# Kernel tuning notes

Measured on AMD Instinct MI355X. Metric: run time of the kernel, lower is better.

The kernel has to match this reference:

```python
import jax, jax.numpy as jnp
import numpy as np

REG_MAX = 16
BOX_W = 7.5
OBJ_W = 1.0
TOPK = 10
EPS = 1e-7


def dfl_decode(x, reg_max):
    # x: [B, 4*reg_max, N] -> expected value of per-side distribution -> [B, N, 4] (xyxy)
    B, C, N = x.shape
    x = x.reshape(B, 4, reg_max, N)
    p = jax.nn.softmax(x, axis=2)
    proj = jnp.arange(reg_max, dtype=x.dtype)
    return jnp.einsum('bkrn,r->bnk', p, proj)


def bbox_ciou(b1, b2):
    # b1: [B,N,1,4], b2: [B,1,M,4], xyxy -> [B,N,M]
    x11, y11, x12, y12 = b1[..., 0], b1[..., 1], b1[..., 2], b1[..., 3]
    x21, y21, x22, y22 = b2[..., 0], b2[..., 1], b2[..., 2], b2[..., 3]
    w1, h1 = x12 - x11, y12 - y11
    w2, h2 = x22 - x21, y22 - y21
    iw = jnp.clip(jnp.minimum(x12, x22) - jnp.maximum(x11, x21), 0.0)
    ih = jnp.clip(jnp.minimum(y12, y22) - jnp.maximum(y11, y21), 0.0)
    inter = iw * ih
    union = w1 * h1 + w2 * h2 - inter + EPS
    iou = inter / union
    cw = jnp.maximum(x12, x22) - jnp.minimum(x11, x21)
    ch = jnp.maximum(y12, y22) - jnp.minimum(y11, y21)
    c2 = cw * cw + ch * ch + EPS
    rho2 = ((x21 + x22 - x11 - x12) ** 2 + (y21 + y22 - y11 - y12) ** 2) * 0.25
    v = (4.0 / (np.pi ** 2)) * (jnp.arctan(w2 / (h2 + EPS)) - jnp.arctan(w1 / (h1 + EPS))) ** 2
    alpha = jax.lax.stop_gradient(v / (v - iou + 1.0 + EPS))
    return iou - rho2 / c2 - alpha * v


def setup_inputs() -> dict:
    key = jax.random.key(0)
    k1, k2, k3, k4 = jax.random.split(key, 4)
    B, N, M = 8, 34000, 64
    boxes = jax.random.normal(k1, (B, 4 * REG_MAX, N), dtype=jnp.float32)
    scores = jax.random.normal(k2, (B, N), dtype=jnp.float32)
    # GT boxes: valid xyxy in roughly the same [0, reg_max) range as decoded preds
    xy = jax.random.uniform(k3, (B, M, 2), dtype=jnp.float32) * 11.0
    wh = jax.random.uniform(k4, (B, M, 2), dtype=jnp.float32) * 4.0 + 0.5
    targets = jnp.concatenate([xy, xy + wh], axis=-1)
    return {'boxes': boxes, 'scores': scores, 'targets': targets}


def reference(boxes, scores, targets):
    B, N = scores.shape
    M = targets.shape[1]
    pb = dfl_decode(boxes, REG_MAX)                     # [B,N,4]
    ciou = bbox_ciou(pb[:, :, None, :], targets[:, None, :, :])  # [B,N,M]
    k = min(TOPK, N)
    topv, topi = jax.lax.top_k(jnp.swapaxes(ciou, 1, 2), k)      # [B,M,k] over anchors
    valid = topv > 0.0
    vals = jnp.where(valid, topv, 0.0)

    def per_batch(idx, val, vld):
        flat_i = idx.reshape(-1)
        iou_t = jnp.zeros((N,), val.dtype).at[flat_i].max(val.reshape(-1))
        pos = jnp.zeros((N,), bool).at[flat_i].max(vld.reshape(-1))
        return iou_t, pos

    iou_target, pos = jax.vmap(per_batch)(topi, vals, valid)     # [B,N]
    posf = pos.astype(iou_target.dtype)
    npos = posf.sum(axis=1)
    box_per = jnp.where(npos > 0,
                        ((1.0 - iou_target) * posf).sum(axis=1) / jnp.maximum(npos, 1.0),
                        0.0)
    box_loss = box_per.sum()
    # BCEWithLogits (mean over anchors), summed over batch
    bce = jnp.maximum(scores, 0.0) - scores * iou_target + jnp.log1p(jnp.exp(-jnp.abs(scores)))
    obj_loss = bce.mean(axis=1).sum()
    total = (BOX_W * box_loss + OBJ_W * obj_loss) / B
    return total, box_loss, obj_loss
```

## Files before the change

### kernel.cpp

```cpp
#include <hip/hip_runtime.h>
#include <math.h>

#define BQ 8
#define MQ 64
#define REGMAX 16
#define KTOP 10
#define EPSQ 1e-7f
#define APB 512
#define MBUF 1024

__device__ __forceinline__ float frcp(float x) { return __builtin_amdgcn_rcpf(x); }

__device__ __forceinline__ float dfl_side(const float* __restrict__ p, size_t Ns) {
  float x0 = p[0];
  float x1 = p[Ns];
  float x2 = p[2 * Ns];
  float x3 = p[3 * Ns];
  float x4 = p[4 * Ns];
  float x5 = p[5 * Ns];
  float x6 = p[6 * Ns];
  float x7 = p[7 * Ns];
  float x8 = p[8 * Ns];
  float x9 = p[9 * Ns];
  float x10 = p[10 * Ns];
  float x11 = p[11 * Ns];
  float x12 = p[12 * Ns];
  float x13 = p[13 * Ns];
  float x14 = p[14 * Ns];
  float x15 = p[15 * Ns];
  float mx = fmaxf(fmaxf(fmaxf(fmaxf(x0, x1), fmaxf(x2, x3)),
                         fmaxf(fmaxf(x4, x5), fmaxf(x6, x7))),
                   fmaxf(fmaxf(fmaxf(x8, x9), fmaxf(x10, x11)),
                         fmaxf(fmaxf(x12, x13), fmaxf(x14, x15))));
  float s = 0.f, ws = 0.f, e;
  e = __expf(x0 - mx); s += e;
  e = __expf(x1 - mx); s += e; ws += 1.f * e;
  e = __expf(x2 - mx); s += e; ws += 2.f * e;
  e = __expf(x3 - mx); s += e; ws += 3.f * e;
  e = __expf(x4 - mx); s += e; ws += 4.f * e;
  e = __expf(x5 - mx); s += e; ws += 5.f * e;
  e = __expf(x6 - mx); s += e; ws += 6.f * e;
  e = __expf(x7 - mx); s += e; ws += 7.f * e;
  e = __expf(x8 - mx); s += e; ws += 8.f * e;
  e = __expf(x9 - mx); s += e; ws += 9.f * e;
  e = __expf(x10 - mx); s += e; ws += 10.f * e;
  e = __expf(x11 - mx); s += e; ws += 11.f * e;
  e = __expf(x12 - mx); s += e; ws += 12.f * e;
  e = __expf(x13 - mx); s += e; ws += 13.f * e;
  e = __expf(x14 - mx); s += e; ws += 14.f * e;
  e = __expf(x15 - mx); s += e; ws += 15.f * e;
  return ws * frcp(s);
}

__device__ __forceinline__ float2 dfl_side2(const float* __restrict__ p, size_t Ns) {
  float2 x0 = *(const float2*)(p);
  float2 x1 = *(const float2*)(p + Ns);
  float2 x2 = *(const float2*)(p + 2 * Ns);
  float2 x3 = *(const float2*)(p + 3 * Ns);
  float2 x4 = *(const float2*)(p + 4 * Ns);
  float2 x5 = *(const float2*)(p + 5 * Ns);
  float2 x6 = *(const float2*)(p + 6 * Ns);
  float2 x7 = *(const float2*)(p + 7 * Ns);
  float2 x8 = *(const float2*)(p + 8 * Ns);
  float2 x9 = *(const float2*)(p + 9 * Ns);
  float2 x10 = *(const float2*)(p + 10 * Ns);
  float2 x11 = *(const float2*)(p + 11 * Ns);
  float2 x12 = *(const float2*)(p + 12 * Ns);
  float2 x13 = *(const float2*)(p + 13 * Ns);
  float2 x14 = *(const float2*)(p + 14 * Ns);
  float2 x15 = *(const float2*)(p + 15 * Ns);
  float mxa = fmaxf(fmaxf(fmaxf(fmaxf(x0.x, x1.x), fmaxf(x2.x, x3.x)),
                          fmaxf(fmaxf(x4.x, x5.x), fmaxf(x6.x, x7.x))),
                    fmaxf(fmaxf(fmaxf(x8.x, x9.x), fmaxf(x10.x, x11.x)),
                          fmaxf(fmaxf(x12.x, x13.x), fmaxf(x14.x, x15.x))));
  float mxb = fmaxf(fmaxf(fmaxf(fmaxf(x0.y, x1.y), fmaxf(x2.y, x3.y)),
                          fmaxf(fmaxf(x4.y, x5.y), fmaxf(x6.y, x7.y))),
                    fmaxf(fmaxf(fmaxf(x8.y, x9.y), fmaxf(x10.y, x11.y)),
                          fmaxf(fmaxf(x12.y, x13.y), fmaxf(x14.y, x15.y))));
  float sa = 0.f, wa = 0.f, sb = 0.f, wb = 0.f, e;
  e = __expf(x0.x - mxa); sa += e;
  e = __expf(x0.y - mxb); sb += e;
  e = __expf(x1.x - mxa); sa += e; wa += 1.f * e;
  e = __expf(x1.y - mxb); sb += e; wb += 1.f * e;
  e = __expf(x2.x - mxa); sa += e; wa += 2.f * e;
  e = __expf(x2.y - mxb); sb += e; wb += 2.f * e;
  e = __expf(x3.x - mxa); sa += e; wa += 3.f * e;
  e = __expf(x3.y - mxb); sb += e; wb += 3.f * e;
  e = __expf(x4.x - mxa); sa += e; wa += 4.f * e;
  e = __expf(x4.y - mxb); sb += e; wb += 4.f * e;
  e = __expf(x5.x - mxa); sa += e; wa += 5.f * e;
  e = __expf(x5.y - mxb); sb += e; wb += 5.f * e;
  e = __expf(x6.x - mxa); sa += e; wa += 6.f * e;
  e = __expf(x6.y - mxb); sb += e; wb += 6.f * e;
  e = __expf(x7.x - mxa); sa += e; wa += 7.f * e;
  e = __expf(x7.y - mxb); sb += e; wb += 7.f * e;
  e = __expf(x8.x - mxa); sa += e; wa += 8.f * e;
  e = __expf(x8.y - mxb); sb += e; wb += 8.f * e;
  e = __expf(x9.x - mxa); sa += e; wa += 9.f * e;
  e = __expf(x9.y - mxb); sb += e; wb += 9.f * e;
  e = __expf(x10.x - mxa); sa += e; wa += 10.f * e;
  e = __expf(x10.y - mxb); sb += e; wb += 10.f * e;
  e = __expf(x11.x - mxa); sa += e; wa += 11.f * e;
  e = __expf(x11.y - mxb); sb += e; wb += 11.f * e;
  e = __expf(x12.x - mxa); sa += e; wa += 12.f * e;
  e = __expf(x12.y - mxb); sb += e; wb += 12.f * e;
  e = __expf(x13.x - mxa); sa += e; wa += 13.f * e;
  e = __expf(x13.y - mxb); sb += e; wb += 13.f * e;
  e = __expf(x14.x - mxa); sa += e; wa += 14.f * e;
  e = __expf(x14.y - mxb); sb += e; wb += 14.f * e;
  e = __expf(x15.x - mxa); sa += e; wa += 15.f * e;
  e = __expf(x15.y - mxb); sb += e; wb += 15.f * e;
  return make_float2(wa * frcp(sa), wb * frcp(sb));
}

__global__ __launch_bounds__(256) void decode_topk_kernel(
    const float* __restrict__ boxes, const float* __restrict__ scores,
    const float* __restrict__ targets, unsigned int* __restrict__ iou_bits,
    uint2* __restrict__ cand, float* __restrict__ bcePartial,
    unsigned int* __restrict__ ctr, int N, int bpb) {
  const int tid = threadIdx.x;
  const int b = blockIdx.x / bpb;
  const int blk = blockIdx.x - b * bpb;
  const int a0 = blk * APB;
  const int w = tid >> 6;
  const int l = tid & 63;

  __shared__ float4 s_sv[APB];
  __shared__ float s_at[APB];
  __shared__ int s_ix[APB];
  __shared__ float s_hv[4 * MQ * KTOP];
  __shared__ int s_hi[4 * MQ * KTOP];
  __shared__ uint2 s_mg[MQ * KTOP];
  __shared__ int s_cnt;
  __shared__ float s_bce;
  if (tid == 0) { s_cnt = 0; s_bce = 0.f; }
  if (blockIdx.x == 0 && tid == 0) *ctr = 0u;
  __syncthreads();

  const int n0 = a0 + 2 * tid;
  float bce0 = 0.f;
  if (n0 < N) {
    const size_t i = (size_t)b * N + n0;
    const size_t Ns = (size_t)N;
    const float* base = boxes + (size_t)(b * 64) * Ns + n0;
    if (n0 + 1 < N) {
      iou_bits[i] = 0u;
      iou_bits[i + 1] = 0u;
      float2 sc = *(const float2*)(scores + i);
      bce0 = fmaxf(sc.x, 0.f) + log1pf(__expf(-fabsf(sc.x))) +
             fmaxf(sc.y, 0.f) + log1pf(__expf(-fabsf(sc.y)));
      float2 ev0 = dfl_side2(base, Ns);
      float2 ev1 = dfl_side2(base + 16 * Ns, Ns);
      float2 ev2 = dfl_side2(base + 32 * Ns, Ns);
      float2 ev3 = dfl_side2(base + 48 * Ns, Ns);
      float w1 = ev2.x - ev0.x, h1 = ev3.x - ev1.x;
      if (w1 > 0.f && h1 > 0.f) {
        int slot = atomicAdd(&s_cnt, 1);
        s_sv[slot] = make_float4(ev0.x, ev1.x, ev2.x, ev3.x);
        s_at[slot] = atanf(w1 * frcp(h1 + EPSQ));
        s_ix[slot] = n0;
      }
      float w1b = ev2.y - ev0.y, h1b = ev3.y - ev1.y;
      if (w1b > 0.f && h1b > 0.f) {
        int slot = atomicAdd(&s_cnt, 1);
        s_sv[slot] = make_float4(ev0.y, ev1.y, ev2.y, ev3.y);
        s_at[slot] = atanf(w1b * frcp(h1b + EPSQ));
        s_ix[slot] = n0 + 1;
      }
    } else {
      iou_bits[i] = 0u;
      float sc = scores[i];
      bce0 = fmaxf(sc, 0.f) + log1pf(__expf(-fabsf(sc)));
      float ev0 = dfl_side(base, Ns);
      float ev1 = dfl_side(base + 16 * Ns, Ns);
      float ev2 = dfl_side(base + 32 * Ns, Ns);
      float ev3 = dfl_side(base + 48 * Ns, Ns);
      float w1 = ev2 - ev0, h1 = ev3 - ev1;
      if (w1 > 0.f && h1 > 0.f) {
        int slot = atomicAdd(&s_cnt, 1);
        s_sv[slot] = make_float4(ev0, ev1, ev2, ev3);
        s_at[slot] = atanf(w1 * frcp(h1 + EPSQ));
        s_ix[slot] = n0;
      }
    }
  }
#pragma unroll
  for (int d = 1; d < 64; d <<= 1) bce0 += __shfl_xor(bce0, d, 64);
  if (l == 0) atomicAdd(&s_bce, bce0);
  __syncthreads();
  const int nsurv = s_cnt;
  if (tid == 0) bcePartial[blockIdx.x] = s_bce;

  const float4 t = ((const float4*)targets)[b * MQ + l];
  const float x21 = t.x, y21 = t.y, x22 = t.z, y22 = t.w;
  const float w2 = x22 - x21, h2 = y22 - y21;
  const float atan_t = atanf(w2 * frcp(h2 + EPSQ));
  const float area2 = w2 * h2, sumx2 = x21 + x22, sumy2 = y21 + y22;
  const float CPI = 4.0f / (float)(M_PI * M_PI);

  float hv0 = 0.f, hv1 = 0.f, hv2 = 0.f, hv3 = 0.f, hv4 = 0.f;
  float hv5 = 0.f, hv6 = 0.f, hv7 = 0.f, hv8 = 0.f, hv9 = 0.f;
  int hi0 = 0, hi1 = 0, hi2 = 0, hi3 = 0, hi4 = 0;
  int hi5 = 0, hi6 = 0, hi7 = 0, hi8 = 0, hi9 = 0;

  const int qlen = (nsurv + 3) >> 2;
  const int j0 = w * qlen;
  const int j1 = min(nsurv, j0 + qlen);
  for (int j = j0; j < j1; ++j) {
    float4 p = s_sv[j];
    float pa = s_at[j];
    int ixj = s_ix[j];
    float x11 = p.x, y11 = p.y, x12 = p.z, y12 = p.w;
    float w1 = x12 - x11, h1 = y12 - y11;
    float iw = fmaxf(fminf(x12, x22) - fmaxf(x11, x21), 0.f);
    float ih = fmaxf(fminf(y12, y22) - fmaxf(y11, y21), 0.f);
    float inter = iw * ih;
    float uni = w1 * h1 + area2 - inter + EPSQ;
    float iou = inter * frcp(uni);
    float cw = fmaxf(x12, x22) - fminf(x11, x21);
    float ch = fmaxf(y12, y22) - fminf(y11, y21);
    float c2 = cw * cw + ch * ch + EPSQ;
    float dx = sumx2 - x11 - x12;
    float dy = sumy2 - y11 - y12;
    float rho2 = (dx * dx + dy * dy) * 0.25f;
    float da = atan_t - pa;
    float v = CPI * da * da;
    float alpha = v * frcp(v - iou + 1.f + EPSQ);
    float ciou = iou - rho2 * frcp(c2) - alpha * v;
    if (ciou > hv9) {
      float cv = ciou;
      int ci = ixj;
#define INS(vk, ik)                         \
  {                                         \
    bool gt = cv > vk;                      \
    float tv_ = vk; int ti_ = ik;           \
    vk = gt ? cv : vk; ik = gt ? ci : ik;   \
    cv = gt ? tv_ : cv; ci = gt ? ti_ : ci; \
  }
      INS(hv0, hi0) INS(hv1, hi1) INS(hv2, hi2) INS(hv3, hi3) INS(hv4, hi4)
      INS(hv5, hi5) INS(hv6, hi6) INS(hv7, hi7) INS(hv8, hi8) INS(hv9, hi9)
#undef INS
    }
  }
  const int hb = (w * MQ + l) * KTOP;
  s_hv[hb + 0] = hv0; s_hi[hb + 0] = hi0;
  s_hv[hb + 1] = hv1; s_hi[hb + 1] = hi1;
  s_hv[hb + 2] = hv2; s_hi[hb + 2] = hi2;
  s_hv[hb + 3] = hv3; s_hi[hb + 3] = hi3;
  s_hv[hb + 4] = hv4; s_hi[hb + 4] = hi4;
  s_hv[hb + 5] = hv5; s_hi[hb + 5] = hi5;
  s_hv[hb + 6] = hv6; s_hi[hb + 6] = hi6;
  s_hv[hb + 7] = hv7; s_hi[hb + 7] = hi7;
  s_hv[hb + 8] = hv8; s_hi[hb + 8] = hi8;
  s_hv[hb + 9] = hv9; s_hi[hb + 9] = hi9;
  __syncthreads();

  if (w == 0) {
    const int m = l;
    int p0 = 0, p1 = 0, p2 = 0, p3 = 0;
    for (int r = 0; r < KTOP; ++r) {
      float c0 = s_hv[(0 * MQ + m) * KTOP + p0];
      float c1 = s_hv[(1 * MQ + m) * KTOP + p1];
      float c2m = s_hv[(2 * MQ + m) * KTOP + p2];
      float c3 = s_hv[(3 * MQ + m) * KTOP + p3];
      float best = c0; int bw = 0;
      if (c1 > best) { best = c1; bw = 1; }
      if (c2m > best) { best = c2m; bw = 2; }
      if (c3 > best) { best = c3; bw = 3; }
      int psel = (bw == 0) ? p0 : (bw == 1) ? p1 : (bw == 2) ? p2 : p3;
      int bidx = s_hi[(bw * MQ + m) * KTOP + psel];
      s_mg[m * KTOP + r] = make_uint2(__float_as_uint(best), (unsigned)bidx);
      if (bw == 0) p0 = min(p0 + 1, KTOP - 1);
      else if (bw == 1) p1 = min(p1 + 1, KTOP - 1);
      else if (bw == 2) p2 = min(p2 + 1, KTOP - 1);
      else p3 = min(p3 + 1, KTOP - 1);
    }
  }
  __syncthreads();
  for (int sl = tid; sl < MQ * KTOP; sl += 256) {
    int m = sl / KTOP;
    int r = sl - m * KTOP;
    cand[((size_t)(b * MQ + m) * bpb + blk) * KTOP + r] = s_mg[sl];
  }
}

__device__ __forceinline__ void select_top10(
    float* s_bv, int* s_bi, float* s_winv, int* s_wini,
    int* s_cnt, int c, int tid) {
  if (tid < 64) {
    for (int r = 0; r < KTOP; ++r) {
      float bv = 0.f;
      int bs = 0xffff;
      for (int sl = tid; sl < c; sl += 64) {
        float v = s_bv[sl];
        if (v > bv) { bv = v; bs = sl; }
      }
      unsigned long long key =
          ((unsigned long long)__float_as_uint(bv) << 32) | (unsigned int)bs;
#pragma unroll
      for (int d = 1; d < 64; d <<= 1) {
        unsigned long long o = __shfl_xor(key, d, 64);
        if (o > key) key = o;
      }
      if (tid == 0) {
        float wv = __uint_as_float((unsigned int)(key >> 32));
        int ws = (int)(key & 0xffffu);
        s_winv[r] = wv;
        if (wv > 0.f && ws != 0xffff) {
          s_wini[r] = s_bi[ws];
          s_bv[ws] = 0.f;
        } else {
          s_wini[r] = 0;
        }
      }
    }
    if (tid < KTOP) { s_bv[tid] = s_winv[tid]; s_bi[tid] = s_wini[tid]; }
    if (tid == 0) *s_cnt = KTOP;
  }
}

__global__ __launch_bounds__(256) void merge_kernel(
    const uint2* __restrict__ cand, const float* __restrict__ scores,
    unsigned int* __restrict__ iou_bits, const float* __restrict__ bcePartial,
    float* __restrict__ mergePartial, unsigned int* __restrict__ ctr,
    float* __restrict__ out, int N, int bpb) {
  const int bm = blockIdx.x;
  const int b = bm >> 6;
  const int tid = threadIdx.x;
  const int NC = bpb * KTOP;

  __shared__ float s_bv[MBUF];
  __shared__ int s_bi[MBUF];
  __shared__ float s_winv[KTOP];
  __shared__ int s_wini[KTOP];
  __shared__ int s_cnt;
  __shared__ float s_d[3];
  __shared__ int s_last;
  __shared__ float s_box[BQ], s_obj[BQ];
  if (tid == 0) s_cnt = 0;
  if (tid < 3) s_d[tid] = 0.f;
  __syncthreads();

  const uint2* cbase = cand + (size_t)bm * NC;
  for (int k2 = tid; k2 < NC; k2 += 256) {
    uint2 e = cbase[k2];
    float v = __uint_as_float(e.x);
    if (v > 0.f) {
      int slot = atomicAdd(&s_cnt, 1);
      s_bv[slot] = v;
      s_bi[slot] = (int)e.y;
    }
  }
  __syncthreads();
  int c = s_cnt;
  __syncthreads();
  if (c > KTOP) {
    select_top10(s_bv, s_bi, s_winv, s_wini, &s_cnt, c, tid);
    __syncthreads();
    c = KTOP;
  }
  if (tid < KTOP && tid < c) {
    float v = s_bv[tid];
    if (v > 0.f) {
      int ix = s_bi[tid];
      unsigned int vb = __float_as_uint(v);
      unsigned int old = atomicMax(&iou_bits[(size_t)b * N + ix], vb);
      if (old < vb) {
        float vold = __uint_as_float(old);
        bool was = (old != 0u);
        atomicAdd(&s_d[0], was ? (vold - v) : (1.f - v));
        if (!was) atomicAdd(&s_d[1], 1.f);
        atomicAdd(&s_d[2], -scores[(size_t)b * N + ix] * (v - vold));
      }
    }
  }
  __syncthreads();
  if (tid == 0) {
    float4* mp = (float4*)(mergePartial + (size_t)bm * 4);
    *mp = make_float4(s_d[0], s_d[1], s_d[2], 0.f);
    __threadfence();
    unsigned int done = atomicAdd(ctr, 1u);
    s_last = (done == (unsigned)(gridDim.x - 1)) ? 1 : 0;
  }
  __syncthreads();
  if (s_last) {
    __threadfence();
    if (tid < BQ) {
      const int bb = tid;
      volatile const float* mp = mergePartial;
      float sbox = 0.f, snp = 0.f, sbce = 0.f;
      for (int mm = 0; mm < MQ; ++mm) {
        int idx = (bb * MQ + mm) * 4;
        sbox += mp[idx];
        snp += mp[idx + 1];
        sbce += mp[idx + 2];
      }
      volatile const float* bp = bcePartial;
      for (int k2 = 0; k2 < bpb; ++k2) sbce += bp[bb * bpb + k2];
      s_box[bb] = (snp > 0.f) ? sbox / fmaxf(snp, 1.f) : 0.f;
      s_obj[bb] = sbce / (float)N;
    }
    __syncthreads();
    if (tid == 0) {
      float box = 0.f, obj = 0.f;
      for (int bb = 0; bb < BQ; ++bb) { box += s_box[bb]; obj += s_obj[bb]; }
      out[0] = (7.5f * box + obj) / (float)BQ;
      out[1] = box;
      out[2] = obj;
    }
  }
}

extern "C" void kernel_launch(void* const* d_in, const int* in_sizes, int n_in,
                              void* d_out, int out_size, void* d_ws, size_t ws_size,
                              hipStream_t stream) {
  const float* boxes = (const float*)d_in[0];
  const float* scores = (const float*)d_in[1];
  const float* targets = (const float*)d_in[2];
  float* out = (float*)d_out;
  const int N = in_sizes[1] / BQ;

  const int bpb = (N + APB - 1) / APB;
  const int nblk = BQ * bpb;

  char* ws = (char*)d_ws;
  size_t cand_bytes = (size_t)BQ * MQ * bpb * KTOP * sizeof(uint2);
  size_t iou_bytes = (size_t)BQ * N * sizeof(unsigned int);
  size_t bce_bytes = (((size_t)nblk * sizeof(float)) + 255) & ~(size_t)255;
  size_t mp_bytes = (size_t)BQ * MQ * 4 * sizeof(float);

  uint2* cand = (uint2*)ws;                    ws += cand_bytes;
  unsigned int* iou_bits = (unsigned int*)ws;  ws += iou_bytes;
  float* bcePartial = (float*)ws;              ws += bce_bytes;
  float* mergePartial = (float*)ws;            ws += mp_bytes;
  unsigned int* ctr = (unsigned int*)ws;

  decode_topk_kernel<<<nblk, 256, 0, stream>>>(boxes, scores, targets,
                                               iou_bits, cand, bcePartial, ctr, N, bpb);
  merge_kernel<<<BQ * MQ, 256, 0, stream>>>(cand, scores, iou_bits, bcePartial,
                                            mergePartial, ctr, out, N, bpb);
}
```

Before: 164.3 us.

## Decode four anchors per thread with float4 loads and parallelize final reduction

Each thread now decodes four consecutive anchors using float4 loads of the DFL logits, which doubles anchors per block and halves the number of blocks and the per-block candidate lists the merge stage scans. The last merge block's final sum over partials is spread across all threads with shared atomics instead of eight serial threads. The trade-off is more registers per thread, which can lower occupancy, plus fewer but heavier blocks and larger top-k candidate sets per block.

New measurement: 159.3 us. 1.03x faster.

```diff
diff --git a/kernel.cpp b/kernel.cpp
--- a/kernel.cpp
+++ b/kernel.cpp
@@ -6,7 +6,7 @@
 #define REGMAX 16
 #define KTOP 10
 #define EPSQ 1e-7f
-#define APB 512
+#define APB 1024
 #define MBUF 1024
 
 __device__ __forceinline__ float frcp(float x) { return __builtin_amdgcn_rcpf(x); }
@@ -52,65 +52,47 @@
   return ws * frcp(s);
 }
 
-__device__ __forceinline__ float2 dfl_side2(const float* __restrict__ p, size_t Ns) {
-  float2 x0 = *(const float2*)(p);
-  float2 x1 = *(const float2*)(p + Ns);
-  float2 x2 = *(const float2*)(p + 2 * Ns);
-  float2 x3 = *(const float2*)(p + 3 * Ns);
-  float2 x4 = *(const float2*)(p + 4 * Ns);
-  float2 x5 = *(const float2*)(p + 5 * Ns);
-  float2 x6 = *(const float2*)(p + 6 * Ns);
-  float2 x7 = *(const float2*)(p + 7 * Ns);
-  float2 x8 = *(const float2*)(p + 8 * Ns);
-  float2 x9 = *(const float2*)(p + 9 * Ns);
-  float2 x10 = *(const float2*)(p + 10 * Ns);
-  float2 x11 = *(const float2*)(p + 11 * Ns);
-  float2 x12 = *(const float2*)(p + 12 * Ns);
-  float2 x13 = *(const float2*)(p + 13 * Ns);
-  float2 x14 = *(const float2*)(p + 14 * Ns);
-  float2 x15 = *(const float2*)(p + 15 * Ns);
-  float mxa = fmaxf(fmaxf(fmaxf(fmaxf(x0.x, x1.x), fmaxf(x2.x, x3.x)),
-                          fmaxf(fmaxf(x4.x, x5.x), fmaxf(x6.x, x7.x))),
-                    fmaxf(fmaxf(fmaxf(x8.x, x9.x), fmaxf(x10.x, x11.x)),
-                          fmaxf(fmaxf(x12.x, x13.x), fmaxf(x14.x, x15.x))));
-  float mxb = fmaxf(fmaxf(fmaxf(fmaxf(x0.y, x1.y), fmaxf(x2.y, x3.y)),
-                          fmaxf(fmaxf(x4.y, x5.y), fmaxf(x6.y, x7.y))),
-                    fmaxf(fmaxf(fmaxf(x8.y, x9.y), fmaxf(x10.y, x11.y)),
-                          fmaxf(fmaxf(x12.y, x13.y), fmaxf(x14.y, x15.y))));
-  float sa = 0.f, wa = 0.f, sb = 0.f, wb = 0.f, e;
-  e = __expf(x0.x - mxa); sa += e;
-  e = __expf(x0.y - mxb); sb += e;
-  e = __expf(x1.x - mxa); sa += e; wa += 1.f * e;
-  e = __expf(x1.y - mxb); sb += e; wb += 1.f * e;
-  e = __expf(x2.x - mxa); sa += e; wa += 2.f * e;
-  e = __expf(x2.y - mxb); sb += e; wb += 2.f * e;
-  e = __expf(x3.x - mxa); sa += e; wa += 3.f * e;
-  e = __expf(x3.y - mxb); sb += e; wb += 3.f * e;
-  e = __expf(x4.x - mxa); sa += e; wa += 4.f * e;
-  e = __expf(x4.y - mxb); sb += e; wb += 4.f * e;
-  e = __expf(x5.x - mxa); sa += e; wa += 5.f * e;
-  e = __expf(x5.y - mxb); sb += e; wb += 5.f * e;
-  e = __expf(x6.x - mxa); sa += e; wa += 6.f * e;
-  e = __expf(x6.y - mxb); sb += e; wb += 6.f * e;
-  e = __expf(x7.x - mxa); sa += e; wa += 7.f * e;
-  e = __expf(x7.y - mxb); sb += e; wb += 7.f * e;
-  e = __expf(x8.x - mxa); sa += e; wa += 8.f * e;
-  e = __expf(x8.y - mxb); sb += e; wb += 8.f * e;
-  e = __expf(x9.x - mxa); sa += e; wa += 9.f * e;
-  e = __expf(x9.y - mxb); sb += e; wb += 9.f * e;
-  e = __expf(x10.x - mxa); sa += e; wa += 10.f * e;
-  e = __expf(x10.y - mxb); sb += e; wb += 10.f * e;
-  e = __expf(x11.x - mxa); sa += e; wa += 11.f * e;
-  e = __expf(x11.y - mxb); sb += e; wb += 11.f * e;
-  e = __expf(x12.x - mxa); sa += e; wa += 12.f * e;
-  e = __expf(x12.y - mxb); sb += e; wb += 12.f * e;
-  e = __expf(x13.x - mxa); sa += e; wa += 13.f * e;
-  e = __expf(x13.y - mxb); sb += e; wb += 13.f * e;
-  e = __expf(x14.x - mxa); sa += e; wa += 14.f * e;
-  e = __expf(x14.y - mxb); sb += e; wb += 14.f * e;
-  e = __expf(x15.x - mxa); sa += e; wa += 15.f * e;
-  e = __expf(x15.y - mxb); sb += e; wb += 15.f * e;
-  return make_float2(wa * frcp(sa), wb * frcp(sb));
+__device__ __forceinline__ float4 dfl_side4(const float* __restrict__ p, size_t Ns) {
+  float4 x0 = *(const float4*)(p);
+  float4 x1 = *(const float4*)(p + Ns);
+  float4 x2 = *(const float4*)(p + 2 * Ns);
+  float4 x3 = *(const float4*)(p + 3 * Ns);
+  float4 x4 = *(const float4*)(p + 4 * Ns);
+  float4 x5 = *(const float4*)(p + 5 * Ns);
+  float4 x6 = *(const float4*)(p + 6 * Ns);
+  float4 x7 = *(const float4*)(p + 7 * Ns);
+  float4 x8 = *(const float4*)(p + 8 * Ns);
+  float4 x9 = *(const float4*)(p + 9 * Ns);
+  float4 x10 = *(const float4*)(p + 10 * Ns);
+  float4 x11 = *(const float4*)(p + 11 * Ns);
+  float4 x12 = *(const float4*)(p + 12 * Ns);
+  float4 x13 = *(const float4*)(p + 13 * Ns);
+  float4 x14 = *(const float4*)(p + 14 * Ns);
+  float4 x15 = *(const float4*)(p + 15 * Ns);
+#define MAX16(c)                                                        \
+  fmaxf(fmaxf(fmaxf(fmaxf(x0.c, x1.c), fmaxf(x2.c, x3.c)),              \
+              fmaxf(fmaxf(x4.c, x5.c), fmaxf(x6.c, x7.c))),             \
+        fmaxf(fmaxf(fmaxf(x8.c, x9.c), fmaxf(x10.c, x11.c)),            \
+              fmaxf(fmaxf(x12.c, x13.c), fmaxf(x14.c, x15.c))))
+  float mxa = MAX16(x);
+  float mxb = MAX16(y);
+  float mxc = MAX16(z);
+  float mxd = MAX16(w);
+#undef MAX16
+  float sa = 0.f, wa = 0.f, sb = 0.f, wb = 0.f;
+  float sc = 0.f, wc = 0.f, sd = 0.f, wd = 0.f;
+  float e;
+#define STEP(K, XK)                                      \
+  e = __expf(XK.x - mxa); sa += e; wa += (float)K * e;   \
+  e = __expf(XK.y - mxb); sb += e; wb += (float)K * e;   \
+  e = __expf(XK.z - mxc); sc += e; wc += (float)K * e;   \
+  e = __expf(XK.w - mxd); sd += e; wd += (float)K * e;
+  STEP(0, x0) STEP(1, x1) STEP(2, x2) STEP(3, x3)
+  STEP(4, x4) STEP(5, x5) STEP(6, x6) STEP(7, x7)
+  STEP(8, x8) STEP(9, x9) STEP(10, x10) STEP(11, x11)
+  STEP(12, x12) STEP(13, x13) STEP(14, x14) STEP(15, x15)
+#undef STEP
+  return make_float4(wa * frcp(sa), wb * frcp(sb), wc * frcp(sc), wd * frcp(sd));
 }
 
 __global__ __launch_bounds__(256) void decode_topk_kernel(
@@ -137,50 +119,50 @@
   if (blockIdx.x == 0 && tid == 0) *ctr = 0u;
   __syncthreads();
 
-  const int n0 = a0 + 2 * tid;
+  auto emit = [&](float e0, float e1, float e2, float e3, int n) {
+    float w1 = e2 - e0, h1 = e3 - e1;
+    if (w1 > 0.f && h1 > 0.f) {
+      int slot = atomicAdd(&s_cnt, 1);
+      s_sv[slot] = make_float4(e0, e1, e2, e3);
+      s_at[slot] = atanf(w1 * frcp(h1 + EPSQ));
+      s_ix[slot] = n;
+    }
+  };
+
+  const int n0 = a0 + 4 * tid;
   float bce0 = 0.f;
   if (n0 < N) {
     const size_t i = (size_t)b * N + n0;
     const size_t Ns = (size_t)N;
     const float* base = boxes + (size_t)(b * 64) * Ns + n0;
-    if (n0 + 1 < N) {
-      iou_bits[i] = 0u;
-      iou_bits[i + 1] = 0u;
-      float2 sc = *(const float2*)(scores + i);
-      bce0 = fmaxf(sc.x, 0.f) + log1pf(__expf(-fabsf(sc.x))) +
-             fmaxf(sc.y, 0.f) + log1pf(__expf(-fabsf(sc.y)));
-      float2 ev0 = dfl_side2(base, Ns);
-      float2 ev1 = dfl_side2(base + 16 * Ns, Ns);
-      float2 ev2 = dfl_side2(base + 32 * Ns, Ns);
-      float2 ev3 = dfl_side2(base + 48 * Ns, Ns);
-      float w1 = ev2.x - ev0.x, h1 = ev3.x - ev1.x;
-      if (w1 > 0.f && h1 > 0.f) {
-        int slot = atomicAdd(&s_cnt, 1);
-        s_sv[slot] = make_float4(ev0.x, ev1.x, ev2.x, ev3.x);
-        s_at[slot] = atanf(w1 * frcp(h1 + EPSQ));
-        s_ix[slot] = n0;
-      }
-      float w1b = ev2.y - ev0.y, h1b = ev3.y - ev1.y;
-      if (w1b > 0.f && h1b > 0.f) {
-        int slot = atomicAdd(&s_cnt, 1);
-        s_sv[slot] = make_float4(ev0.y, ev1.y, ev2.y, ev3.y);
-        s_at[slot] = atanf(w1b * frcp(h1b + EPSQ));
-        s_ix[slot] = n0 + 1;
-      }
+    if ((N & 3) == 0 && n0 + 3 < N) {
+      *(uint4*)(iou_bits + i) = make_uint4(0u, 0u, 0u, 0u);
+      float4 sc4 = *(const float4*)(scores + i);
+      bce0 = fmaxf(sc4.x, 0.f) + log1pf(__expf(-fabsf(sc4.x))) +
+             fmaxf(sc4.y, 0.f) + log1pf(__expf(-fabsf(sc4.y))) +
+             fmaxf(sc4.z, 0.f) + log1pf(__expf(-fabsf(sc4.z))) +
+             fmaxf(sc4.w, 0.f) + log1pf(__expf(-fabsf(sc4.w)));
+      float4 ev0 = dfl_side4(base, Ns);
+      float4 ev1 = dfl_side4(base + 16 * Ns, Ns);
+      float4 ev2 = dfl_side4(base + 32 * Ns, Ns);
+      float4 ev3 = dfl_side4(base + 48 * Ns, Ns);
+      emit(ev0.x, ev1.x, ev2.x, ev3.x, n0 + 0);
+      emit(ev0.y, ev1.y, ev2.y, ev3.y, n0 + 1);
+      emit(ev0.z, ev1.z, ev2.z, ev3.z, n0 + 2);
+      emit(ev0.w, ev1.w, ev2.w, ev3.w, n0 + 3);
     } else {
-      iou_bits[i] = 0u;
-      float sc = scores[i];
-      bce0 = fmaxf(sc, 0.f) + log1pf(__expf(-fabsf(sc)));
-      float ev0 = dfl_side(base, Ns);
-      float ev1 = dfl_side(base + 16 * Ns, Ns);
-      float ev2 = dfl_side(base + 32 * Ns, Ns);
-      float ev3 = dfl_side(base + 48 * Ns, Ns);
-      float w1 = ev2 - ev0, h1 = ev3 - ev1;
-      if (w1 > 0.f && h1 > 0.f) {
-        int slot = atomicAdd(&s_cnt, 1);
-        s_sv[slot] = make_float4(ev0, ev1, ev2, ev3);
-        s_at[slot] = atanf(w1 * frcp(h1 + EPSQ));
-        s_ix[slot] = n0;
+      for (int k = 0; k < 4; ++k) {
+        int n = n0 + k;
+        if (n >= N) break;
+        iou_bits[i + k] = 0u;
+        float sc = scores[i + k];
+        bce0 += fmaxf(sc, 0.f) + log1pf(__expf(-fabsf(sc)));
+        const float* bp = base + k;
+        float ev0 = dfl_side(bp, Ns);
+        float ev1 = dfl_side(bp + 16 * Ns, Ns);
+        float ev2 = dfl_side(bp + 32 * Ns, Ns);
+        float ev3 = dfl_side(bp + 48 * Ns, Ns);
+        emit(ev0, ev1, ev2, ev3, n);
       }
     }
   }
@@ -336,9 +318,10 @@
   __shared__ int s_cnt;
   __shared__ float s_d[3];
   __shared__ int s_last;
-  __shared__ float s_box[BQ], s_obj[BQ];
+  __shared__ float s_acc[BQ * 3];
   if (tid == 0) s_cnt = 0;
   if (tid < 3) s_d[tid] = 0.f;
+  if (tid < BQ * 3) s_acc[tid] = 0.f;
   __syncthreads();
 
   const uint2* cbase = cand + (size_t)bm * NC;
@@ -385,25 +368,29 @@
   __syncthreads();
   if (s_last) {
     __threadfence();
-    if (tid < BQ) {
-      const int bb = tid;
-      volatile const float* mp = mergePartial;
-      float sbox = 0.f, snp = 0.f, sbce = 0.f;
-      for (int mm = 0; mm < MQ; ++mm) {
-        int idx = (bb * MQ + mm) * 4;
-        sbox += mp[idx];
-        snp += mp[idx + 1];
-        sbce += mp[idx + 2];
-      }
-      volatile const float* bp = bcePartial;
-      for (int k2 = 0; k2 < bpb; ++k2) sbce += bp[bb * bpb + k2];
-      s_box[bb] = (snp > 0.f) ? sbox / fmaxf(snp, 1.f) : 0.f;
-      s_obj[bb] = sbce / (float)N;
+    volatile const float* mp = mergePartial;
+    for (int i = tid; i < BQ * MQ; i += 256) {
+      int bb = i >> 6;
+      float a0 = mp[i * 4 + 0];
+      float a1 = mp[i * 4 + 1];
+      float a2 = mp[i * 4 + 2];
+      atomicAdd(&s_acc[bb * 3 + 0], a0);
+      atomicAdd(&s_acc[bb * 3 + 1], a1);
+      atomicAdd(&s_acc[bb * 3 + 2], a2);
+    }
+    volatile const float* bp = bcePartial;
+    for (int i = tid; i < BQ * bpb; i += 256) {
+      int bb = i / bpb;
+      atomicAdd(&s_acc[bb * 3 + 2], bp[i]);
     }
     __syncthreads();
     if (tid == 0) {
       float box = 0.f, obj = 0.f;
-      for (int bb = 0; bb < BQ; ++bb) { box += s_box[bb]; obj += s_obj[bb]; }
+      for (int bb = 0; bb < BQ; ++bb) {
+        float np = s_acc[bb * 3 + 1];
+        box += (np > 0.f) ? s_acc[bb * 3 + 0] / fmaxf(np, 1.f) : 0.f;
+        obj += s_acc[bb * 3 + 2] / (float)N;
+      }
       out[0] = (7.5f * box + obj) / (float)BQ;
       out[1] = box;
       out[2] = obj;
```
